# Kernel optimization log

Measured on AMD Instinct MI355X. Metric: run time of the kernel, lower is better.

Reference implementation:

```python
import jax, jax.numpy as jnp
import numpy as np

B, S, DIM = 2, 2048, 2048
NH = 16
D_NOPE, D_ROPE, D_V = 128, 64, 128
D_QK = D_NOPE + D_ROPE  # 192
KV_RANK = 512
RMS_EPS = 1e-6


def setup_inputs() -> dict:
    key = jax.random.key(0)
    ks = jax.random.split(key, 8)
    x = jax.random.normal(ks[0], (B, S, DIM), dtype=jnp.float32)
    # rotary freqs as (cos, sin) pairs: [S, D_ROPE//2, 2]
    pos = jnp.arange(S, dtype=jnp.float32)
    inv_freq = 1.0 / (10000.0 ** (jnp.arange(0, D_ROPE, 2, dtype=jnp.float32) / D_ROPE))
    ang = pos[:, None] * inv_freq[None, :]
    freqs_cis = jnp.stack([jnp.cos(ang), jnp.sin(ang)], axis=-1)
    # causal mask [S, S]
    mask = jnp.where(jnp.arange(S)[None, :] > jnp.arange(S)[:, None], -jnp.inf, 0.0).astype(jnp.float32)
    sd = lambda k, shp, fan: jax.random.normal(k, shp, dtype=jnp.float32) * (fan ** -0.5)
    wq = sd(ks[1], (NH * D_QK, DIM), DIM)
    wkv_a = sd(ks[2], (KV_RANK + D_ROPE, DIM), DIM)
    wkv_b = sd(ks[3], (NH * (D_NOPE + D_V), KV_RANK), KV_RANK)
    wo = sd(ks[4], (DIM, NH * D_V), NH * D_V)
    kv_norm_w = jnp.ones((KV_RANK,), dtype=jnp.float32)
    return {"x": x, "start_pos": 0, "freqs_cis": freqs_cis, "mask": mask,
            "wq": wq, "wkv_a": wkv_a, "wkv_b": wkv_b, "wo": wo, "kv_norm_w": kv_norm_w}


def _rope(x, freqs):
    # x: [b, s, h, d] with d even; freqs: [s, d//2, 2] (cos, sin)
    b, s, h, d = x.shape
    xr = x.reshape(b, s, h, d // 2, 2)
    cos = freqs[None, :, None, :, 0]
    sin = freqs[None, :, None, :, 1]
    ye = xr[..., 0] * cos - xr[..., 1] * sin
    yo = xr[..., 0] * sin + xr[..., 1] * cos
    return jnp.stack([ye, yo], axis=-1).reshape(b, s, h, d)


def _rms_norm(x, w):
    var = jnp.mean(jnp.square(x), axis=-1, keepdims=True)
    return x * jax.lax.rsqrt(var + RMS_EPS) * w


def reference(x, start_pos, freqs_cis, mask, wq, wkv_a, wkv_b, wo, kv_norm_w):
    b, s, _ = x.shape
    scale = D_QK ** -0.5
    # query projection -> [b, s, h, d_qk]
    q = jnp.einsum('bsd,ed->bse', x, wq).reshape(b, s, NH, D_QK)
    q_nope, q_pe = q[..., :D_NOPE], q[..., D_NOPE:]
    q_pe = _rope(q_pe, freqs_cis)
    q = jnp.concatenate([q_nope, q_pe], axis=-1)
    # latent kv projection -> [b, s, kv_rank + d_rope]
    kv = jnp.einsum('bsd,ed->bse', x, wkv_a)
    kv_lat, k_pe = kv[..., :KV_RANK], kv[..., KV_RANK:]
    k_pe = _rope(k_pe[:, :, None, :], freqs_cis)  # [b, s, 1, d_rope]
    kv_up = jnp.einsum('bsr,er->bse', _rms_norm(kv_lat, kv_norm_w), wkv_b)
    kv_up = kv_up.reshape(b, s, NH, D_NOPE + D_V)
    k_nope, v = kv_up[..., :D_NOPE], kv_up[..., D_NOPE:]
    k = jnp.concatenate([k_nope, jnp.broadcast_to(k_pe, (b, s, NH, D_ROPE))], axis=-1)
    # start_pos = 0 prefill: cache[:end_pos] == freshly computed k, v
    scores = jnp.einsum('bshd,bthd->bsht', q, k) * scale
    if mask is not None:
        scores = scores + mask[None, :, None, :]
    probs = jax.nn.softmax(scores.astype(jnp.float32), axis=-1).astype(x.dtype)
    out = jnp.einsum('bsht,bthd->bshd', probs, v)
    return jnp.einsum('bse,de->bsd', out.reshape(b, s, NH * D_V), wo)
```

## Files before the change

kernel.cpp:

```cpp
#include <hip/hip_runtime.h>
#include <hip/hip_bf16.h>


typedef __bf16 bf16x8 __attribute__((ext_vector_type(8)));
typedef float  f32x4  __attribute__((ext_vector_type(4)));
typedef float  f32x16 __attribute__((ext_vector_type(16)));
typedef unsigned short us8 __attribute__((ext_vector_type(8)));
typedef unsigned short us4 __attribute__((ext_vector_type(4)));
typedef unsigned int   ui4 __attribute__((ext_vector_type(4)));

#define S_LEN   2048
#define BS_TOT  4096
#define NH      16
#define DQK     192
#define DV      128
#define KV_RANK 512
#define QSTR    3712

__device__ inline unsigned short f2bf(float f) {
  __hip_bfloat16 h = __float2bfloat16(f);
  return *reinterpret_cast<unsigned short*>(&h);
}
__device__ inline float bfu2f(unsigned short u) {
  unsigned int x = ((unsigned int)u) << 16;
  return __builtin_bit_cast(float, x);
}
__device__ inline unsigned int pack2bf(float a, float b) {
  return (unsigned int)f2bf(a) | ((unsigned int)f2bf(b) << 16);
}
__device__ inline void glds16(const void* g, void* l) {
  __builtin_amdgcn_global_load_lds(
      (const __attribute__((address_space(1))) unsigned int*)g,
      (__attribute__((address_space(3))) unsigned int*)l, 16, 0, 0);
}

__global__ __launch_bounds__(256) void cast_all_kernel(
    const float* __restrict__ x, const float* __restrict__ wq,
    const float* __restrict__ wkva, const float* __restrict__ wkvb,
    const float* __restrict__ wo,
    __hip_bfloat16* __restrict__ xb, __hip_bfloat16* __restrict__ wqb,
    __hip_bfloat16* __restrict__ wkvab, __hip_bfloat16* __restrict__ wkvbb,
    __hip_bfloat16* __restrict__ wob) {
  const int bid = blockIdx.x;
  const float* src; __hip_bfloat16* dst; int n, npad, b0, nb;
  if (bid < 771)       { src = x;    dst = xb;    n = 8388608; npad = 8388608; b0 = 0;    nb = 771; }
  else if (bid < 1349) { src = wq;   dst = wqb;   n = 6291456; npad = 6291456; b0 = 771;  nb = 578; }
  else if (bid < 1469) { src = wkva; dst = wkvab; n = 1179648; npad = 1310720; b0 = 1349; nb = 120; }
  else if (bid < 1662) { src = wkvb; dst = wkvbb; n = 2097152; npad = 2097152; b0 = 1469; nb = 193; }
  else                 { src = wo;   dst = wob;   n = 4194304; npad = 4194304; b0 = 1662; nb = 386; }
  const int tid = (bid - b0) * 256 + threadIdx.x;
  const int stride = nb * 256;
  for (int i = tid * 4; i < npad; i += stride * 4) {
    if (i + 3 < n) {
      f32x4 v = *(const f32x4*)(src + i);
      dst[i + 0] = __float2bfloat16(v.x);
      dst[i + 1] = __float2bfloat16(v.y);
      dst[i + 2] = __float2bfloat16(v.z);
      dst[i + 3] = __float2bfloat16(v.w);
    } else {
#pragma unroll
      for (int z = 0; z < 4; z++)
        dst[i + z] = __float2bfloat16((i + z < n) ? src[i + z] : 0.f);
    }
  }
}

template<int OUT_BF16>
__global__ __launch_bounds__(256) void gemm_bt(const __hip_bfloat16* __restrict__ A,
                                               const __hip_bfloat16* __restrict__ Bw,
                                               void* __restrict__ Cp,
                                               int M, int N, int K) {
  constexpr int BM = 128, BN = 128, BK = 32;
  __shared__ alignas(16) unsigned short As[BM * BK];
  __shared__ alignas(16) unsigned short Bs[BN * BK];
  const int tid  = threadIdx.x;
  const int m0   = blockIdx.y * BM, n0 = blockIdx.x * BN;
  const int w    = tid >> 6, lane = tid & 63;
  const int wm   = (w >> 1) * 64, wn = (w & 1) * 64;
  const int ml   = lane & 15, quad = lane >> 4;
  const int srow = w * 16 + (lane >> 2);
  const int scol = (lane & 3) * 8;

  f32x4 acc[4][4];
#pragma unroll
  for (int i = 0; i < 4; i++)
#pragma unroll
    for (int j = 0; j < 4; j++)
#pragma unroll
      for (int e = 0; e < 4; e++) acc[i][j][e] = 0.0f;

  const unsigned short* Ag = (const unsigned short*)A;
  const unsigned short* Bg = (const unsigned short*)Bw;
  const unsigned short* a0 = Ag + (size_t)(m0 + srow) * K + scol;
  const unsigned short* a1 = Ag + (size_t)(m0 + srow + 64) * K + scol;
  const unsigned short* b0 = Bg + (size_t)(n0 + srow) * K + scol;
  const unsigned short* b1 = Bg + (size_t)(n0 + srow + 64) * K + scol;
  unsigned short* lA0 = &As[(w * 16) * BK];
  unsigned short* lA1 = &As[(64 + w * 16) * BK];
  unsigned short* lB0 = &Bs[(w * 16) * BK];
  unsigned short* lB1 = &Bs[(64 + w * 16) * BK];

  for (int k0 = 0; k0 < K; k0 += BK) {
    __syncthreads();
    glds16(a0 + k0, lA0);
    glds16(a1 + k0, lA1);
    glds16(b0 + k0, lB0);
    glds16(b1 + k0, lB1);
    __syncthreads();

    bf16x8 af[4], bfr[4];
#pragma unroll
    for (int mi = 0; mi < 4; mi++)
      af[mi] = *(const bf16x8*)&As[(wm + mi * 16 + ml) * BK + quad * 8];
#pragma unroll
    for (int ni = 0; ni < 4; ni++)
      bfr[ni] = *(const bf16x8*)&Bs[(wn + ni * 16 + ml) * BK + quad * 8];
#pragma unroll
    for (int mi = 0; mi < 4; mi++)
#pragma unroll
      for (int ni = 0; ni < 4; ni++)
        acc[mi][ni] = __builtin_amdgcn_mfma_f32_16x16x32_bf16(af[mi], bfr[ni],
                                                              acc[mi][ni], 0, 0, 0);
  }

#pragma unroll
  for (int mi = 0; mi < 4; mi++) {
#pragma unroll
    for (int ni = 0; ni < 4; ni++) {
      int col = n0 + wn + ni * 16 + ml;
      if (col < N) {
#pragma unroll
        for (int j = 0; j < 4; j++) {
          int row = m0 + wm + mi * 16 + quad * 4 + j;
          float v = acc[mi][ni][j];
          if (OUT_BF16)
            ((__hip_bfloat16*)Cp)[(size_t)row * N + col] = __float2bfloat16(v);
          else
            ((float*)Cp)[(size_t)row * N + col] = v;
        }
      }
    }
  }
}

__global__ __launch_bounds__(256) void rope_q_kernel(__hip_bfloat16* __restrict__ q,
                                                     const float* __restrict__ freqs) {
  int si = blockIdx.x;
  int s  = si & (S_LEN - 1);
  int tid = threadIdx.x;
  for (int p = tid; p < NH * 32; p += 256) {
    int h = p >> 5, i = p & 31;
    size_t base = (size_t)si * QSTR + h * DQK + 128 + 2 * i;
    float c  = freqs[s * 64 + 2 * i];
    float sn = freqs[s * 64 + 2 * i + 1];
    float x0 = __bfloat162float(q[base]);
    float x1 = __bfloat162float(q[base + 1]);
    q[base]     = __float2bfloat16(x0 * c - x1 * sn);
    q[base + 1] = __float2bfloat16(x0 * sn + x1 * c);
  }
}

__global__ __launch_bounds__(256) void rms_rope_kv_kernel(
    const __hip_bfloat16* __restrict__ qkv, const float* __restrict__ w,
    const float* __restrict__ freqs, __hip_bfloat16* __restrict__ latent,
    __hip_bfloat16* __restrict__ kpe_out) {
  int si = blockIdx.x;
  int tid = threadIdx.x;
  const unsigned short* row = (const unsigned short*)qkv + (size_t)si * QSTR + 3072;
  float v0 = bfu2f(row[tid]), v1 = bfu2f(row[tid + 256]);
  float ss = v0 * v0 + v1 * v1;
#pragma unroll
  for (int off = 1; off < 64; off <<= 1) ss += __shfl_xor(ss, off, 64);
  __shared__ float red[4];
  if ((tid & 63) == 0) red[tid >> 6] = ss;
  __syncthreads();
  float tot = red[0] + red[1] + red[2] + red[3];
  float r = rsqrtf(tot / 512.0f + 1e-6f);
  latent[(size_t)si * 512 + tid]       = __float2bfloat16(v0 * r * w[tid]);
  latent[(size_t)si * 512 + tid + 256] = __float2bfloat16(v1 * r * w[tid + 256]);
  if (tid < 32) {
    int s = si & (S_LEN - 1);
    float c  = freqs[s * 64 + 2 * tid];
    float sn = freqs[s * 64 + 2 * tid + 1];
    float x0 = bfu2f(row[512 + 2 * tid]), x1 = bfu2f(row[512 + 2 * tid + 1]);
    kpe_out[(size_t)si * 64 + 2 * tid]     = __float2bfloat16(x0 * c - x1 * sn);
    kpe_out[(size_t)si * 64 + 2 * tid + 1] = __float2bfloat16(x0 * sn + x1 * c);
  }
}

__global__ __launch_bounds__(512, 2) void attn_mfma_kernel(
    const __hip_bfloat16* __restrict__ qb,
    const __hip_bfloat16* __restrict__ kvup,
    const __hip_bfloat16* __restrict__ kpe,
    unsigned short* __restrict__ op0,
    unsigned short* __restrict__ op1,
    float* __restrict__ mlp0,
    float* __restrict__ mlp1) {
  constexpr int KS = 200;
  constexpr int VS = 36;
  __shared__ alignas(16) unsigned short Ks[2][64 * KS];
  __shared__ alignas(16) unsigned int   Vt2[2][128 * VS];

  const int id = blockIdx.x;
  const int x  = id >> 5;
  const int hb = id & 31;
  const int h  = hb >> 1, b = hb & 1;

  const int tid = threadIdx.x, wave = tid >> 6, lane = tid & 63;
  const int l31 = lane & 31, hh = lane >> 5;
  const float qs2 = 0.07216878364870322f * 1.4426950408889634f;

  const int m16 = tid & 15;
  const int hp  = tid >> 4;
  const int vkey = (m16 & 7) << 2;
  const unsigned short* kvbase = (const unsigned short*)kvup;
  const unsigned short* kpbase = (const unsigned short*)kpe;

#pragma unroll 1
  for (int item = 0; item < 2; ++item) {
    const int qt2    = item ? (7 - x) : x;
    const int kstart = item ? (2 * qt2 + 2) : 0;
    const int kend   = kstart + 2 * qt2 + 2;
    const int qwb = qt2 * 256 + wave * 32;
    const int qg  = qwb + l31;

    bf16x8 Qf[12];
    {
      const unsigned short* qrow = (const unsigned short*)qb +
          (size_t)(b * S_LEN + qg) * QSTR + h * DQK;
#pragma unroll
      for (int s = 0; s < 12; s++)
        Qf[s] = *(const bf16x8*)(qrow + s * 16 + hh * 8);
    }

    float m_i = -1e30f, l_i = 0.0f;
    f32x16 O2[4];
#pragma unroll
    for (int mt = 0; mt < 4; mt++)
#pragma unroll
      for (int j = 0; j < 16; j++) O2[mt][j] = 0.0f;

    us8 Kpre[3], Vpre[2];

    if (item) __syncthreads();

    {
      const int kb0 = kstart * 64;
#pragma unroll
      for (int it = 0; it < 3; it++) {
        int slot = tid + it * 512;
        int r = slot / 24, c = slot - r * 24;
        size_t grow = (size_t)(b * S_LEN + kb0 + r);
        Kpre[it] = (c < 16)
            ? *(const us8*)(kvbase + grow * (NH * 256) + h * 256 + c * 8)
            : *(const us8*)(kpbase + grow * 64 + (c - 16) * 8);
      }
      const unsigned short* v0 = kvbase +
          (size_t)(b * S_LEN + kb0 + 2 * hp) * (NH * 256) + h * 256 + 128 + m16 * 8;
      Vpre[0] = *(const us8*)v0;
      Vpre[1] = *(const us8*)(v0 + NH * 256);
#pragma unroll
      for (int it = 0; it < 3; it++) {
        int slot = tid + it * 512;
        int r = slot / 24, c = slot - r * 24;
        *(us8*)&Ks[0][r * KS + c * 8] = Kpre[it];
      }
#pragma unroll
      for (int z = 0; z < 8; z++) {
        int d = m16 * 8 + z;
        Vt2[0][d * VS + (hp ^ vkey)] =
            (unsigned)(unsigned short)Vpre[0][z] |
            ((unsigned)(unsigned short)Vpre[1][z] << 16);
      }
      __syncthreads();
    }

    int cur = 0;
    for (int kt = kstart; kt < kend; kt++) {
      const int kb = kt * 64;
      const unsigned short* ksc = Ks[cur];
      const unsigned int*   vtc = Vt2[cur];

      const int havenext = (kt + 1 < kend);
      if (havenext) {
        const int kb2 = kb + 64;
#pragma unroll
        for (int it = 0; it < 3; it++) {
          int slot = tid + it * 512;
          int r = slot / 24, c = slot - r * 24;
          size_t grow = (size_t)(b * S_LEN + kb2 + r);
          Kpre[it] = (c < 16)
              ? *(const us8*)(kvbase + grow * (NH * 256) + h * 256 + c * 8)
              : *(const us8*)(kpbase + grow * 64 + (c - 16) * 8);
        }
        const unsigned short* v0 = kvbase +
            (size_t)(b * S_LEN + kb2 + 2 * hp) * (NH * 256) + h * 256 + 128 + m16 * 8;
        Vpre[0] = *(const us8*)v0;
        Vpre[1] = *(const us8*)(v0 + NH * 256);
      }

      if (kb <= qwb + 31) {
        f32x16 st2[2];
        __builtin_amdgcn_s_setprio(1);
#pragma unroll
        for (int mt = 0; mt < 2; mt++) {
          f32x16 acc;
#pragma unroll
          for (int j = 0; j < 16; j++) acc[j] = 0.0f;
#pragma unroll
          for (int s = 0; s < 12; s++) {
            bf16x8 kf = *(const bf16x8*)&ksc[(mt * 32 + l31) * KS + s * 16 + hh * 8];
            acc = __builtin_amdgcn_mfma_f32_32x32x16_bf16(kf, Qf[s], acc, 0, 0, 0);
          }
          st2[mt] = acc;
        }
        __builtin_amdgcn_s_setprio(0);

        float mloc = -1e30f;
        if (kb + 64 <= qwb) {
#pragma unroll
          for (int mt = 0; mt < 2; mt++)
#pragma unroll
            for (int r = 0; r < 16; r++) {
              float s = st2[mt][r] * qs2;
              st2[mt][r] = s;
              mloc = fmaxf(mloc, s);
            }
        } else {
#pragma unroll
          for (int mt = 0; mt < 2; mt++)
#pragma unroll
            for (int r = 0; r < 16; r++) {
              int kpos = kb + mt * 32 + (r & 3) + 8 * (r >> 2) + 4 * hh;
              float s = st2[mt][r] * qs2;
              s = (kpos > qg) ? -1e30f : s;
              st2[mt][r] = s;
              mloc = fmaxf(mloc, s);
            }
        }
        mloc = fmaxf(mloc, __shfl_xor(mloc, 32, 64));
        if (!__all(mloc <= m_i + 8.0f)) {
          float m_new = fmaxf(m_i, mloc);
          float alpha = exp2f(m_i - m_new);
          l_i *= alpha;
#pragma unroll
          for (int mt = 0; mt < 4; mt++)
#pragma unroll
            for (int j = 0; j < 16; j++) O2[mt][j] *= alpha;
          m_i = m_new;
        }
        float psum = 0.0f;
#pragma unroll
        for (int mt = 0; mt < 2; mt++)
#pragma unroll
          for (int r = 0; r < 16; r++) {
            float p = exp2f(st2[mt][r] - m_i);
            st2[mt][r] = p;
            psum += p;
          }
        psum += __shfl_xor(psum, 32, 64);
        l_i += psum;

        bf16x8 pf[4];
#pragma unroll
        for (int ss = 0; ss < 4; ss++) {
          const int pmt = ss >> 1, gg = ss & 1;
          unsigned int U0 = pack2bf(st2[pmt][gg * 8 + 0], st2[pmt][gg * 8 + 1]);
          unsigned int U1 = pack2bf(st2[pmt][gg * 8 + 2], st2[pmt][gg * 8 + 3]);
          unsigned int U2 = pack2bf(st2[pmt][gg * 8 + 4], st2[pmt][gg * 8 + 5]);
          unsigned int U3 = pack2bf(st2[pmt][gg * 8 + 6], st2[pmt][gg * 8 + 7]);
          unsigned int E0 = __shfl_xor(hh ? U0 : U2, 32, 64);
          unsigned int E1 = __shfl_xor(hh ? U1 : U3, 32, 64);
          ui4 pd;
          pd.x = hh ? E0 : U0;
          pd.y = hh ? E1 : U1;
          pd.z = hh ? U2 : E0;
          pd.w = hh ? U3 : E1;
          pf[ss] = __builtin_bit_cast(bf16x8, pd);
        }

        __builtin_amdgcn_s_setprio(1);
#pragma unroll
        for (int ss = 0; ss < 4; ss++) {
#pragma unroll
          for (int mt = 0; mt < 4; mt++) {
            int v = mt * 32 + l31;
            const unsigned int* vp =
                &vtc[v * VS + ((ss * 8 + hh * 4) ^ (((v >> 3) & 7) << 2))];
            bf16x8 bv = *(const bf16x8*)vp;
            O2[mt] = __builtin_amdgcn_mfma_f32_32x32x16_bf16(bv, pf[ss], O2[mt],
                                                             0, 0, 0);
          }
        }
        __builtin_amdgcn_s_setprio(0);
      }

      if (havenext) {
#pragma unroll
        for (int it = 0; it < 3; it++) {
          int slot = tid + it * 512;
          int r = slot / 24, c = slot - r * 24;
          *(us8*)&Ks[cur ^ 1][r * KS + c * 8] = Kpre[it];
        }
#pragma unroll
        for (int z = 0; z < 8; z++) {
          int d = m16 * 8 + z;
          Vt2[cur ^ 1][d * VS + (hp ^ vkey)] =
              (unsigned)(unsigned short)Vpre[0][z] |
              ((unsigned)(unsigned short)Vpre[1][z] << 16);
        }
        __syncthreads();
        cur ^= 1;
      }
    }

    unsigned short* op = item ? op1 : op0;
    float* mlp = item ? mlp1 : mlp0;
    const size_t basep = (size_t)(b * S_LEN + qg) * NH + h;
    unsigned short* orow = op + basep * 128;
#pragma unroll
    for (int mt = 0; mt < 4; mt++) {
#pragma unroll
      for (int g = 0; g < 4; g++) {
        us4 pk;
#pragma unroll
        for (int j = 0; j < 4; j++) pk[j] = f2bf(O2[mt][g * 4 + j]);
        *(us4*)(orow + mt * 32 + g * 8 + hh * 4) = pk;
      }
    }
    if (hh == 0) {
      mlp[basep * 2 + 0] = m_i;
      mlp[basep * 2 + 1] = l_i;
    }
  }
}

__global__ __launch_bounds__(256) void attn_combine_kernel(
    const unsigned short* __restrict__ op0, const unsigned short* __restrict__ op1,
    const float* __restrict__ mlp0, const float* __restrict__ mlp1,
    __hip_bfloat16* __restrict__ attn_out) {
  const int bs = blockIdx.x;
  const int tid = threadIdx.x;
  const int h = tid >> 4, dc = (tid & 15) * 8;
  const size_t basep = (size_t)bs * NH + h;
  const us8 a = *(const us8*)(op0 + basep * 128 + dc);
  const us8 c = *(const us8*)(op1 + basep * 128 + dc);
  const float m0 = mlp0[basep * 2], l0 = mlp0[basep * 2 + 1];
  const float m1 = mlp1[basep * 2], l1 = mlp1[basep * 2 + 1];
  const float m = fmaxf(m0, m1);
  const float a0 = exp2f(m0 - m), a1 = exp2f(m1 - m);
  const float inv = 1.0f / (l0 * a0 + l1 * a1);
  us8 o;
#pragma unroll
  for (int z = 0; z < 8; z++) {
    float v = (bfu2f((unsigned short)a[z]) * a0 +
               bfu2f((unsigned short)c[z]) * a1) * inv;
    o[z] = f2bf(v);
  }
  *(us8*)((unsigned short*)attn_out + (size_t)bs * (NH * DV) + h * DV + dc) = o;
}

extern "C" void kernel_launch(void* const* d_in, const int* in_sizes, int n_in,
                              void* d_out, int out_size, void* d_ws, size_t ws_size,
                              hipStream_t stream) {
  const float* x     = (const float*)d_in[0];
  const float* freqs = (const float*)d_in[2];
  const float* wq    = (const float*)d_in[4];
  const float* wkva  = (const float*)d_in[5];
  const float* wkvb  = (const float*)d_in[6];
  const float* wo    = (const float*)d_in[7];
  const float* kvnw  = (const float*)d_in[8];
  float* out = (float*)d_out;

  char* ws = (char*)d_ws;
  size_t off = 0;
  auto alloc = [&](size_t bytes) {
    void* p = ws + off;
    off += (bytes + 255) & ~(size_t)255;
    return p;
  };
  __hip_bfloat16* x_bf    = (__hip_bfloat16*)alloc((size_t)BS_TOT * 2048 * 2);
  __hip_bfloat16* wq_bf   = (__hip_bfloat16*)alloc((size_t)3072 * 2048 * 2);
  __hip_bfloat16* wkva_bf = (__hip_bfloat16*)alloc((size_t)640 * 2048 * 2);
  __hip_bfloat16* wkvb_bf = (__hip_bfloat16*)alloc((size_t)4096 * 512 * 2);
  __hip_bfloat16* wo_bf   = (__hip_bfloat16*)alloc((size_t)2048 * 2048 * 2);
  __hip_bfloat16* qkv_bf  = (__hip_bfloat16*)alloc((size_t)BS_TOT * QSTR * 2);
  __hip_bfloat16* latent  = (__hip_bfloat16*)alloc((size_t)BS_TOT * 512 * 2);
  __hip_bfloat16* kpe     = (__hip_bfloat16*)alloc((size_t)BS_TOT * 64 * 2);
  __hip_bfloat16* kvup    = (__hip_bfloat16*)alloc((size_t)BS_TOT * 4096 * 2);
  __hip_bfloat16* attn    = (__hip_bfloat16*)alloc((size_t)BS_TOT * 2048 * 2);

  unsigned short* op0 = (unsigned short*)x_bf;
  unsigned short* op1 = (unsigned short*)wq_bf;
  float* mlp0 = (float*)latent;
  float* mlp1 = mlp0 + (size_t)BS_TOT * NH * 2;

  cast_all_kernel<<<2048, 256, 0, stream>>>(x, wq, wkva, wkvb, wo,
                                            x_bf, wq_bf, wkva_bf, wkvb_bf, wo_bf);

  gemm_bt<1><<<dim3(QSTR / 128, BS_TOT / 128), 256, 0, stream>>>(
      x_bf, wq_bf, qkv_bf, BS_TOT, QSTR, 2048);
  rope_q_kernel<<<BS_TOT, 256, 0, stream>>>(qkv_bf, freqs);
  rms_rope_kv_kernel<<<BS_TOT, 256, 0, stream>>>(qkv_bf, kvnw, freqs, latent, kpe);

  gemm_bt<1><<<dim3(4096 / 128, BS_TOT / 128), 256, 0, stream>>>(
      latent, wkvb_bf, kvup, BS_TOT, 4096, 512);

  attn_mfma_kernel<<<dim3(256, 1, 1), 512, 0, stream>>>(
      qkv_bf, kvup, kpe, op0, op1, mlp0, mlp1);
  attn_combine_kernel<<<dim3(BS_TOT, 1, 1), 256, 0, stream>>>(
      op0, op1, mlp0, mlp1, attn);

  gemm_bt<0><<<dim3(2048 / 128, BS_TOT / 128), 256, 0, stream>>>(
      attn, wo_bf, out, BS_TOT, 2048, 2048);
}
```

Baseline: 303.7 us.

## Replace 128x128 GEMM with 256x256 double-buffered swizzled tile kernel

Replaces the GEMM with a 512-thread 256x256x64 kernel. It double-buffers LDS loads through global_load_lds with vmcnt-based waits, XOR-swizzles LDS addresses to avoid bank conflicts, raises MFMA priority with setprio, and remaps block ids with an XCD-aware index. The Q/KV output stride is padded to 3840 so N divides 256, which means padding the wkv_a bf16 buffer with zeros. The aim is more data reuse per tile and latency hidden behind compute. The trade-off is fewer blocks (128 for the output GEMM on a 256-CU part) and higher LDS and register pressure.

```diff
diff --git a/kernel.cpp b/kernel.cpp
--- a/kernel.cpp
+++ b/kernel.cpp
@@ -15,7 +15,7 @@
 #define DQK     192
 #define DV      128
 #define KV_RANK 512
-#define QSTR    3712
+#define QSTR    3840
 
 __device__ inline unsigned short f2bf(float f) {
   __hip_bfloat16 h = __float2bfloat16(f);
@@ -45,7 +45,7 @@
   const float* src; __hip_bfloat16* dst; int n, npad, b0, nb;
   if (bid < 771)       { src = x;    dst = xb;    n = 8388608; npad = 8388608; b0 = 0;    nb = 771; }
   else if (bid < 1349) { src = wq;   dst = wqb;   n = 6291456; npad = 6291456; b0 = 771;  nb = 578; }
-  else if (bid < 1469) { src = wkva; dst = wkvab; n = 1179648; npad = 1310720; b0 = 1349; nb = 120; }
+  else if (bid < 1469) { src = wkva; dst = wkvab; n = 1179648; npad = 1572864; b0 = 1349; nb = 120; }
   else if (bid < 1662) { src = wkvb; dst = wkvbb; n = 2097152; npad = 2097152; b0 = 1469; nb = 193; }
   else                 { src = wo;   dst = wob;   n = 4194304; npad = 4194304; b0 = 1662; nb = 386; }
   const int tid = (bid - b0) * 256 + threadIdx.x;
@@ -66,78 +66,121 @@
 }
 
 template<int OUT_BF16>
-__global__ __launch_bounds__(256) void gemm_bt(const __hip_bfloat16* __restrict__ A,
-                                               const __hip_bfloat16* __restrict__ Bw,
-                                               void* __restrict__ Cp,
-                                               int M, int N, int K) {
-  constexpr int BM = 128, BN = 128, BK = 32;
-  __shared__ alignas(16) unsigned short As[BM * BK];
-  __shared__ alignas(16) unsigned short Bs[BN * BK];
-  const int tid  = threadIdx.x;
-  const int m0   = blockIdx.y * BM, n0 = blockIdx.x * BN;
-  const int w    = tid >> 6, lane = tid & 63;
-  const int wm   = (w >> 1) * 64, wn = (w & 1) * 64;
-  const int ml   = lane & 15, quad = lane >> 4;
-  const int srow = w * 16 + (lane >> 2);
-  const int scol = (lane & 3) * 8;
-
-  f32x4 acc[4][4];
-#pragma unroll
-  for (int i = 0; i < 4; i++)
+__global__ __launch_bounds__(512, 2) void gemm_bt256(
+    const __hip_bfloat16* __restrict__ A, const __hip_bfloat16* __restrict__ Bw,
+    void* __restrict__ Cp, int M, int N, int K, int nbx) {
+  __shared__ alignas(16) unsigned short Asl[2][256 * 64];
+  __shared__ alignas(16) unsigned short Bsl[2][256 * 64];
+
+  const int nwg = gridDim.x;
+  const int cpx = nwg >> 3;
+  const int id  = (blockIdx.x & 7) * cpx + (blockIdx.x >> 3);
+  const int bx = id % nbx, by = id / nbx;
+  const int m0 = by * 256, n0 = bx * 256;
+
+  const int tid = threadIdx.x, w = tid >> 6, lane = tid & 63;
+  const int wr = w >> 2, wc = w & 3;
+  const int ml = lane & 15, quad = lane >> 4;
+  const int srow = w * 8 + (lane >> 3);
+  const int scol = ((lane & 7) ^ (lane >> 3)) * 8;
+
+  const unsigned short* Ag = (const unsigned short*)A + (size_t)(m0 + srow) * K + scol;
+  const unsigned short* Bg = (const unsigned short*)Bw + (size_t)(n0 + srow) * K + scol;
+
+  f32x4 acc[8][4];
+#pragma unroll
+  for (int i = 0; i < 8; i++)
 #pragma unroll
     for (int j = 0; j < 4; j++)
 #pragma unroll
       for (int e = 0; e < 4; e++) acc[i][j][e] = 0.0f;
 
-  const unsigned short* Ag = (const unsigned short*)A;
-  const unsigned short* Bg = (const unsigned short*)Bw;
-  const unsigned short* a0 = Ag + (size_t)(m0 + srow) * K + scol;
-  const unsigned short* a1 = Ag + (size_t)(m0 + srow + 64) * K + scol;
-  const unsigned short* b0 = Bg + (size_t)(n0 + srow) * K + scol;
-  const unsigned short* b1 = Bg + (size_t)(n0 + srow + 64) * K + scol;
-  unsigned short* lA0 = &As[(w * 16) * BK];
-  unsigned short* lA1 = &As[(64 + w * 16) * BK];
-  unsigned short* lB0 = &Bs[(w * 16) * BK];
-  unsigned short* lB1 = &Bs[(64 + w * 16) * BK];
-
-  for (int k0 = 0; k0 < K; k0 += BK) {
-    __syncthreads();
-    glds16(a0 + k0, lA0);
-    glds16(a1 + k0, lA1);
-    glds16(b0 + k0, lB0);
-    glds16(b1 + k0, lB1);
-    __syncthreads();
-
-    bf16x8 af[4], bfr[4];
-#pragma unroll
-    for (int mi = 0; mi < 4; mi++)
-      af[mi] = *(const bf16x8*)&As[(wm + mi * 16 + ml) * BK + quad * 8];
-#pragma unroll
-    for (int ni = 0; ni < 4; ni++)
-      bfr[ni] = *(const bf16x8*)&Bs[(wn + ni * 16 + ml) * BK + quad * 8];
-#pragma unroll
-    for (int mi = 0; mi < 4; mi++)
-#pragma unroll
-      for (int ni = 0; ni < 4; ni++)
-        acc[mi][ni] = __builtin_amdgcn_mfma_f32_16x16x32_bf16(af[mi], bfr[ni],
-                                                              acc[mi][ni], 0, 0, 0);
-  }
-
-#pragma unroll
-  for (int mi = 0; mi < 4; mi++) {
+  auto stage = [&](int slot, int k0) {
+#pragma unroll
+    for (int j = 0; j < 4; j++)
+      glds16(Ag + (size_t)j * 64 * K + k0, &Asl[slot][(j * 64 + w * 8) * 64]);
+#pragma unroll
+    for (int j = 0; j < 4; j++)
+      glds16(Bg + (size_t)j * 64 * K + k0, &Bsl[slot][(j * 64 + w * 8) * 64]);
+  };
+
+  const int nt = K / 64;
+  stage(0, 0);
+  stage(1, 64);
+  asm volatile("s_waitcnt vmcnt(8)" ::: "memory");
+  __builtin_amdgcn_s_barrier();
+  asm volatile("" ::: "memory");
+
+  int slot = 0;
+  for (int t = 0; t < nt; ++t) {
+    const unsigned short* As = &Asl[slot][0];
+    const unsigned short* Bs = &Bsl[slot][0];
+
+    bf16x8 bfr[2][2][2];
+#pragma unroll
+    for (int nh = 0; nh < 2; nh++)
+#pragma unroll
+      for (int nf = 0; nf < 2; nf++) {
+        int r = wc * 64 + nh * 32 + nf * 16 + ml;
+        const char* rowp = (const char*)&Bs[r * 64];
+#pragma unroll
+        for (int ks = 0; ks < 2; ks++)
+          bfr[nh][nf][ks] =
+              *(const bf16x8*)(rowp + ((ks * 64 + quad * 16) ^ ((ml & 7) << 4)));
+      }
+#pragma unroll
+    for (int mh = 0; mh < 2; mh++) {
+      bf16x8 af[4][2];
+#pragma unroll
+      for (int mf = 0; mf < 4; mf++) {
+        int r = wr * 128 + mh * 64 + mf * 16 + ml;
+        const char* rowp = (const char*)&As[r * 64];
+#pragma unroll
+        for (int ks = 0; ks < 2; ks++)
+          af[mf][ks] =
+              *(const bf16x8*)(rowp + ((ks * 64 + quad * 16) ^ ((ml & 7) << 4)));
+      }
+      __builtin_amdgcn_s_setprio(1);
+#pragma unroll
+      for (int nh = 0; nh < 2; nh++)
+#pragma unroll
+        for (int mf = 0; mf < 4; mf++)
+#pragma unroll
+          for (int nf = 0; nf < 2; nf++)
+#pragma unroll
+            for (int ks = 0; ks < 2; ks++)
+              acc[mh * 4 + mf][nh * 2 + nf] = __builtin_amdgcn_mfma_f32_16x16x32_bf16(
+                  af[mf][ks], bfr[nh][nf][ks], acc[mh * 4 + mf][nh * 2 + nf], 0, 0, 0);
+      __builtin_amdgcn_s_setprio(0);
+    }
+
+    asm volatile("" ::: "memory");
+    __builtin_amdgcn_s_barrier();
+    asm volatile("" ::: "memory");
+    if (t + 2 < nt) {
+      stage(slot, (t + 2) * 64);
+      asm volatile("s_waitcnt vmcnt(8)" ::: "memory");
+    } else {
+      asm volatile("s_waitcnt vmcnt(0)" ::: "memory");
+    }
+    __builtin_amdgcn_s_barrier();
+    asm volatile("" ::: "memory");
+    slot ^= 1;
+  }
+
+#pragma unroll
+  for (int mi = 0; mi < 8; mi++) {
 #pragma unroll
     for (int ni = 0; ni < 4; ni++) {
-      int col = n0 + wn + ni * 16 + ml;
-      if (col < N) {
-#pragma unroll
-        for (int j = 0; j < 4; j++) {
-          int row = m0 + wm + mi * 16 + quad * 4 + j;
-          float v = acc[mi][ni][j];
-          if (OUT_BF16)
-            ((__hip_bfloat16*)Cp)[(size_t)row * N + col] = __float2bfloat16(v);
-          else
-            ((float*)Cp)[(size_t)row * N + col] = v;
-        }
+      int col = n0 + wc * 64 + ni * 16 + ml;
+      int rowb = m0 + wr * 128 + mi * 16 + quad * 4;
+#pragma unroll
+      for (int j = 0; j < 4; j++) {
+        float v = acc[mi][ni][j];
+        if (OUT_BF16)
+          ((__hip_bfloat16*)Cp)[(size_t)(rowb + j) * N + col] = __float2bfloat16(v);
+        else
+          ((float*)Cp)[(size_t)(rowb + j) * N + col] = v;
       }
     }
   }
@@ -481,7 +524,7 @@
   };
   __hip_bfloat16* x_bf    = (__hip_bfloat16*)alloc((size_t)BS_TOT * 2048 * 2);
   __hip_bfloat16* wq_bf   = (__hip_bfloat16*)alloc((size_t)3072 * 2048 * 2);
-  __hip_bfloat16* wkva_bf = (__hip_bfloat16*)alloc((size_t)640 * 2048 * 2);
+  __hip_bfloat16* wkva_bf = (__hip_bfloat16*)alloc((size_t)768 * 2048 * 2);
   __hip_bfloat16* wkvb_bf = (__hip_bfloat16*)alloc((size_t)4096 * 512 * 2);
   __hip_bfloat16* wo_bf   = (__hip_bfloat16*)alloc((size_t)2048 * 2048 * 2);
   __hip_bfloat16* qkv_bf  = (__hip_bfloat16*)alloc((size_t)BS_TOT * QSTR * 2);
@@ -498,19 +541,19 @@
   cast_all_kernel<<<2048, 256, 0, stream>>>(x, wq, wkva, wkvb, wo,
                                             x_bf, wq_bf, wkva_bf, wkvb_bf, wo_bf);
 
-  gemm_bt<1><<<dim3(QSTR / 128, BS_TOT / 128), 256, 0, stream>>>(
-      x_bf, wq_bf, qkv_bf, BS_TOT, QSTR, 2048);
+  gemm_bt256<1><<<dim3(240), 512, 0, stream>>>(
+      x_bf, wq_bf, qkv_bf, BS_TOT, QSTR, 2048, QSTR / 256);
   rope_q_kernel<<<BS_TOT, 256, 0, stream>>>(qkv_bf, freqs);
   rms_rope_kv_kernel<<<BS_TOT, 256, 0, stream>>>(qkv_bf, kvnw, freqs, latent, kpe);
 
-  gemm_bt<1><<<dim3(4096 / 128, BS_TOT / 128), 256, 0, stream>>>(
-      latent, wkvb_bf, kvup, BS_TOT, 4096, 512);
+  gemm_bt256<1><<<dim3(256), 512, 0, stream>>>(
+      latent, wkvb_bf, kvup, BS_TOT, 4096, 512, 16);
 
   attn_mfma_kernel<<<dim3(256, 1, 1), 512, 0, stream>>>(
       qkv_bf, kvup, kpe, op0, op1, mlp0, mlp1);
   attn_combine_kernel<<<dim3(BS_TOT, 1, 1), 256, 0, stream>>>(
       op0, op1, mlp0, mlp1, attn);
 
-  gemm_bt<0><<<dim3(2048 / 128, BS_TOT / 128), 256, 0, stream>>>(
-      attn, wo_bf, out, BS_TOT, 2048, 2048);
-}
+  gemm_bt256<0><<<dim3(128), 512, 0, stream>>>(
+      attn, wo_bf, out, BS_TOT, 2048, 2048, 8);
+}
```

Result: faster. 266.1 us (-12.4%).
